# Performance work log

Hardware: AMD Instinct MI355X
Metric: run time of the kernel (lower is better)

Reference implementation:

```python
import jax, jax.numpy as jnp
import numpy as np

N, E = 20000, 320000
IN, OUT, H1, H2 = 256, 32, 8, 1
NEG_SLOPE = 0.2


def _gatv2(x, src, dst, Wsrc, bsrc, Wdst, bdst, attn, Wres, bres, heads, dout):
    n = x.shape[0]
    fs = (x @ Wsrc + bsrc).reshape(n, heads, dout)   # (N,H,D)
    fd = (x @ Wdst + bdst).reshape(n, heads, dout)   # (N,H,D)
    # GATv2: leaky_relu BEFORE the attention dot product
    e = jax.nn.leaky_relu(fs[src] + fd[dst], NEG_SLOPE)      # (E,H,D)
    logits = jnp.einsum('ehd,hd->eh', e, attn)               # (E,H)
    # edge softmax over destination-node segments
    m = jax.ops.segment_max(logits, dst, num_segments=n)     # (N,H)
    ex = jnp.exp(logits - m[dst])
    s = jax.ops.segment_sum(ex, dst, num_segments=n)         # (N,H)
    alpha = ex / s[dst]                                      # (E,H)
    msg = alpha[:, :, None] * fs[src]                        # (E,H,D)
    out = jax.ops.segment_sum(msg, dst, num_segments=n)      # (N,H,D)
    res = (x @ Wres + bres).reshape(n, heads, dout)          # residual (dims differ -> Linear)
    return out + res


def setup_inputs() -> dict:
    key = jax.random.key(0)
    ks = jax.random.split(key, 16)
    sc = lambda fin: 1.0 / np.sqrt(fin)
    d = {}
    d['x'] = jax.random.normal(ks[0], (N, IN), jnp.float32)
    d['src'] = jax.random.randint(ks[1], (E,), 0, N, jnp.int32)
    d['dst'] = jax.random.randint(ks[2], (E,), 0, N, jnp.int32)
    # layer 1: IN -> OUT*H1
    d['Wsrc1'] = jax.random.normal(ks[3], (IN, OUT * H1), jnp.float32) * sc(IN)
    d['bsrc1'] = jnp.zeros((OUT * H1,), jnp.float32)
    d['Wdst1'] = jax.random.normal(ks[4], (IN, OUT * H1), jnp.float32) * sc(IN)
    d['bdst1'] = jnp.zeros((OUT * H1,), jnp.float32)
    d['attn1'] = jax.random.normal(ks[5], (H1, OUT), jnp.float32) * sc(OUT)
    d['Wres1'] = jax.random.normal(ks[6], (IN, OUT * H1), jnp.float32) * sc(IN)
    d['bres1'] = jnp.zeros((OUT * H1,), jnp.float32)
    # layer 2: OUT*H1 -> OUT, 1 head
    D2 = OUT * H1
    d['Wsrc2'] = jax.random.normal(ks[7], (D2, OUT * H2), jnp.float32) * sc(D2)
    d['bsrc2'] = jnp.zeros((OUT * H2,), jnp.float32)
    d['Wdst2'] = jax.random.normal(ks[8], (D2, OUT * H2), jnp.float32) * sc(D2)
    d['bdst2'] = jnp.zeros((OUT * H2,), jnp.float32)
    d['attn2'] = jax.random.normal(ks[9], (H2, OUT), jnp.float32) * sc(OUT)
    d['Wres2'] = jax.random.normal(ks[10], (D2, OUT * H2), jnp.float32) * sc(D2)
    d['bres2'] = jnp.zeros((OUT * H2,), jnp.float32)
    return d


def reference(x, src, dst,
              Wsrc1, bsrc1, Wdst1, bdst1, attn1, Wres1, bres1,
              Wsrc2, bsrc2, Wdst2, bdst2, attn2, Wres2, bres2):
    y = _gatv2(x, src, dst, Wsrc1, bsrc1, Wdst1, bdst1, attn1, Wres1, bres1, H1, OUT)
    y = jax.nn.relu(y)                       # (N, 8, OUT)
    y = y.reshape(x.shape[0], -1)            # (N, 8*OUT)
    y = _gatv2(y, src, dst, Wsrc2, bsrc2, Wdst2, bdst2, attn2, Wres2, bres2, H2, OUT)
    return y                                  # (N, 1, OUT)
```

## Files before the change

### kernel.cpp

```cpp
#include <hip/hip_runtime.h>
#include <hip/hip_bf16.h>

#define N_NODES 20000
#define N_PAD   20096
#define N_EDGES 320000
#define D_IN    256
#define NEG     0.2f
#define MAXDEG  64
#define NSB     64
#define EPSB    5000
#define NBIN    313
#define LOG2E   1.4426950408889634f

typedef __attribute__((ext_vector_type(8))) short short8;
typedef __attribute__((ext_vector_type(4))) float f32x4;
typedef __attribute__((ext_vector_type(4))) unsigned short u16x4;

__device__ __forceinline__ unsigned short f2b(float f) {
    unsigned int u = __float_as_uint(f);
    unsigned int r = (u + 0x7FFFu + ((u >> 16) & 1u)) >> 16;
    return (unsigned short)r;
}
__device__ __forceinline__ float b2f(unsigned short u) {
    union { unsigned int i; float f; } v;
    v.i = ((unsigned int)u) << 16;
    return v.f;
}

__device__ __forceinline__ void gload16(const void* g, void* l) {
    __builtin_amdgcn_global_load_lds((const __attribute__((address_space(1))) void*)g,
                                     (__attribute__((address_space(3))) void*)l, 16, 0, 0);
}

#define PB1 2512
#define PB1B 2560
#define PB2 2656
#define PB3 2720
#define PREP_BLOCKS 2768
__global__ __launch_bounds__(256) void k_prep(
    const float* __restrict__ x, unsigned short* __restrict__ xb,
    const float* __restrict__ Ws1, const float* __restrict__ Wd1, const float* __restrict__ Wr1,
    unsigned short* __restrict__ wt,
    const float* __restrict__ Ws2, const float* __restrict__ Wd2, const float* __restrict__ Wr2,
    unsigned short* __restrict__ wt2,
    const int* __restrict__ dst, int* __restrict__ blockhist,
    unsigned short* __restrict__ yb)
{
    __shared__ float tl[64][65];
    __shared__ int hist[NBIN];
    int bid = blockIdx.x, tid = threadIdx.x;
    if (bid < PB1) {
        int i = bid * 256 + tid;
        int row = i >> 5, c8 = (i & 31) * 8;
        short8 v = {0, 0, 0, 0, 0, 0, 0, 0};
        if (row < N_NODES) {
            float4 a = *reinterpret_cast<const float4*>(x + (size_t)row * 256 + c8);
            float4 b = *reinterpret_cast<const float4*>(x + (size_t)row * 256 + c8 + 4);
            v[0] = (short)f2b(a.x); v[1] = (short)f2b(a.y); v[2] = (short)f2b(a.z); v[3] = (short)f2b(a.w);
            v[4] = (short)f2b(b.x); v[5] = (short)f2b(b.y); v[6] = (short)f2b(b.z); v[7] = (short)f2b(b.w);
        }
        *reinterpret_cast<short8*>(xb + (size_t)row * 256 + c8) = v;
    } else if (bid < PB1B) {
        int b = bid - PB1;
        int mat = b >> 4, tile = b & 15;
        int r0 = (tile >> 2) * 64;
        int c0 = (tile & 3) * 64;
        const float* W = (mat == 0) ? Ws1 : ((mat == 1) ? Wd1 : Wr1);
        int lane = tid & 63, grp = tid >> 6;
#pragma unroll
        for (int pass = 0; pass < 16; ++pass) {
            int kl = pass * 4 + grp;
            tl[kl][lane] = W[(size_t)(r0 + kl) * 256 + c0 + lane];
        }
        __syncthreads();
#pragma unroll
        for (int pass = 0; pass < 16; ++pass) {
            int nl = pass * 4 + grp;
            wt[(size_t)(mat * 256 + c0 + nl) * 256 + r0 + lane] = f2b(tl[lane][nl]);
        }
    } else if (bid < PB2) {
        int n = bid - PB1B, k = tid;
        const float* W = (n < 32) ? Ws2 : ((n < 64) ? Wd2 : Wr2);
        int c = n & 31;
        wt2[(size_t)n * 256 + (k ^ ((n & 7) << 3))] = f2b(W[(size_t)k * 32 + c]);
    } else if (bid < PB3) {
        int blk = bid - PB2;
        for (int b = tid; b < NBIN; b += 256) hist[b] = 0;
        __syncthreads();
        for (int it = 0; it < 20; ++it) {
            int li = it * 256 + tid;
            if (li < EPSB) atomicAdd(&hist[dst[blk * EPSB + li] >> 6], 1);
        }
        __syncthreads();
        for (int b = tid; b < NBIN; b += 256) blockhist[blk * NBIN + b] = hist[b];
    } else {
        int j = (bid - PB3) * 256 + tid;
        ((unsigned int*)(yb + (size_t)N_NODES * 256))[j] = 0u;
    }
}

__global__ __launch_bounds__(320) void k_pass3(
    const int* __restrict__ src, const int* __restrict__ dst,
    const int* __restrict__ blockhist,
    unsigned long long* __restrict__ sorted,
    int* __restrict__ binbase_g, int* __restrict__ bintotal_g)
{
    __shared__ int tmp[320];
    __shared__ int binbase[NBIN];
    __shared__ int rank[NBIN];
    int blk = blockIdx.x, tid = threadIdx.x;
    int mystart = 0, total = 0;
    if (tid < NBIN) {
        for (int b = 0; b < NSB; ++b) {
            int v = blockhist[b * NBIN + tid];
            total += v;
            if (b < blk) mystart += v;
        }
    }
    tmp[tid] = (tid < NBIN) ? total : 0;
    __syncthreads();
    for (int off = 1; off < 320; off <<= 1) {
        int v = (tid >= off) ? tmp[tid - off] : 0;
        __syncthreads();
        tmp[tid] += v;
        __syncthreads();
    }
    if (tid < NBIN) {
        int excl = tmp[tid] - total;
        binbase[tid] = excl;
        rank[tid] = mystart;
        if (blk == 0) { binbase_g[tid] = excl; bintotal_g[tid] = total; }
    }
    __syncthreads();
    for (int it = 0; it < 16; ++it) {
        int li = it * 320 + tid;
        if (li < EPSB) {
            int e = blk * EPSB + li;
            int d = dst[e];
            int b = d >> 6;
            int r = atomicAdd(&rank[b], 1);
            sorted[binbase[b] + r] = ((unsigned long long)(unsigned)d << 32) | (unsigned)src[e];
        }
    }
}

#define GEMM1_BLOCKS 1884
#define PASS4_BLOCKS 313
__global__ __launch_bounds__(256) void k_gemm_l1_mfma(
    const unsigned short* __restrict__ xb,
    const unsigned short* __restrict__ wt,
    const float* __restrict__ bs, const float* __restrict__ bd, const float* __restrict__ br,
    unsigned short* __restrict__ fs, unsigned short* __restrict__ fd, unsigned short* __restrict__ res,
    const unsigned long long* __restrict__ sorted,
    const int* __restrict__ binbase_g, const int* __restrict__ bintotal_g,
    int* __restrict__ colp, int* __restrict__ cnt)
{
    __shared__ __align__(16) unsigned short SH[12288];
    int t = threadIdx.x;
    int bid = blockIdx.x;

    if (bid >= GEMM1_BLOCKS) {
        int* ch = (int*)SH;
        int nb2 = bid - GEMM1_BLOCKS;
        if (t < 64) ch[t] = 0;
        __syncthreads();
        int base = binbase_g[nb2], tot = bintotal_g[nb2];
        for (int i = t; i < tot; i += 256) {
            unsigned long long p = sorted[base + i];
            int d = (int)(p >> 32);
            int s = (int)(p & 0xffffffffULL);
            int r = atomicAdd(&ch[d & 63], 1);
            if (r < MAXDEG) colp[(size_t)d * MAXDEG + r] = s;
        }
        __syncthreads();
        int node = nb2 * 64 + t;
        if (t < 64 && node < N_NODES) cnt[node] = ch[t];
        return;
    }

    int lane = t & 63, w = t >> 6;
    const int q = 235, r = 4;
    int xcd = bid & 7, slot = bid >> 3;
    int wg = (xcd < r ? xcd * (q + 1) : r * (q + 1) + (xcd - r) * q) + slot;
    int mb = wg / 6, nb = wg % 6;
    int row0 = mb * 64;
    int which = nb >> 1;
    int col0 = (nb & 1) * 128;
    int ncol0 = nb * 128;
    unsigned short* out = (which == 0) ? fs : ((which == 1) ? fd : res);
    const float* bias   = (which == 0) ? bs : ((which == 1) ? bd : br);

    auto stage = [&](int buf, int k0) {
        char* base = (char*)SH + buf * 12288;
        {
            int c = t, row = c >> 2, kc = (c & 3) * 8;
            gload16(xb + (size_t)(row0 + row) * 256 + k0 + kc, base + c * 16);
        }
#pragma unroll
        for (int r2 = 0; r2 < 2; r2++) {
            int c = r2 * 256 + t, row = c >> 2, kc = (c & 3) * 8;
            gload16(wt + (size_t)(ncol0 + row) * 256 + k0 + kc, base + 4096 + c * 16);
        }
    };

    f32x4 acc[4][2] = {};

    stage(0, 0);
    __syncthreads();
    int cur = 0;
#pragma unroll
    for (int it = 0; it < 8; ++it) {
        if (it < 7) stage(cur ^ 1, (it + 1) * 32);
        const char* Ab = (const char*)SH + cur * 12288;
        const char* Bb = Ab + 4096;
        short8 a[4], b[2];
#pragma unroll
        for (int m = 0; m < 4; m++)
            a[m] = *reinterpret_cast<const short8*>(Ab + ((m * 16 + (lane & 15)) * 64 + (lane >> 4) * 16));
#pragma unroll
        for (int n = 0; n < 2; n++)
            b[n] = *reinterpret_cast<const short8*>(Bb + ((w * 32 + n * 16 + (lane & 15)) * 64 + (lane >> 4) * 16));
#pragma unroll
        for (int m = 0; m < 4; m++)
#pragma unroll
            for (int n = 0; n < 2; n++)
                acc[m][n] = __builtin_amdgcn_mfma_f32_16x16x32_bf16(a[m], b[n], acc[m][n], 0, 0, 0);
        __syncthreads();
        cur ^= 1;
    }

    int cgrp = lane >> 4, ccol = lane & 15;
    float bvals[2];
#pragma unroll
    for (int n = 0; n < 2; n++) bvals[n] = bias[col0 + w * 32 + n * 16 + ccol];

#pragma unroll
    for (int m = 0; m < 4; m++)
#pragma unroll
        for (int n = 0; n < 2; n++)
#pragma unroll
            for (int q2 = 0; q2 < 4; q2++) {
                int lr = m * 16 + cgrp * 4 + q2;
                int cb = (w * 32 + n * 16 + ccol) * 2;
                int addr = lr * 256 + (cb ^ (cgrp << 5));
                *(unsigned short*)((char*)SH + addr) = f2b(acc[m][n][q2] + bvals[n]);
            }
    __syncthreads();
#pragma unroll
    for (int it = 0; it < 4; it++) {
        int lr = it * 16 + (t >> 4);
        int cb = (t & 15) * 16;
        short8 v = *(const short8*)((const char*)SH + (lr * 256 + (cb ^ (((lr >> 2) & 3) << 5))));
        int gr = row0 + lr;
        if (gr < N_NODES)
            *reinterpret_cast<short8*>(out + (size_t)gr * 256 + col0 + (t & 15) * 8) = v;
    }
}

__global__ __launch_bounds__(64) void k_gather_l1(
    const int* __restrict__ cnt, const int* __restrict__ colp,
    const unsigned short* __restrict__ fs1, const unsigned short* __restrict__ fd1,
    const unsigned short* __restrict__ res1, const float* __restrict__ attn1,
    unsigned short* __restrict__ y)
{
    __shared__ int slds[MAXDEG + 8];
    int n = blockIdx.x;
    int l = threadIdx.x;
    int deg = cnt[n];
    if (deg > MAXDEG) deg = MAXDEG;
    slds[l] = (l < deg) ? colp[(size_t)n * MAXDEG + l] : 0;
    if (l < 8) slds[MAXDEG + l] = 0;
    __syncthreads();

    u16x4 fdv4 = *reinterpret_cast<const u16x4*>(fd1 + (size_t)n * 256 + l * 4);
    float fdv[4] = {b2f(fdv4[0]), b2f(fdv4[1]), b2f(fdv4[2]), b2f(fdv4[3])};
    float4 attv = *reinterpret_cast<const float4*>(attn1 + l * 4);
    float att[4] = {attv.x * LOG2E, attv.y * LOG2E, attv.z * LOG2E, attv.w * LOG2E};

    float mA = -1e30f, sA = 0.f, aA0 = 0.f, aA1 = 0.f, aA2 = 0.f, aA3 = 0.f;
    float mB = -1e30f, sB = 0.f, aB0 = 0.f, aB1 = 0.f, aB2 = 0.f, aB3 = 0.f;

    u16x4 fA  = *reinterpret_cast<const u16x4*>(fs1 + (size_t)slds[0] * 256 + l * 4);
    u16x4 fB  = *reinterpret_cast<const u16x4*>(fs1 + (size_t)slds[1] * 256 + l * 4);
    u16x4 fA2 = *reinterpret_cast<const u16x4*>(fs1 + (size_t)slds[2] * 256 + l * 4);
    u16x4 fB2 = *reinterpret_cast<const u16x4*>(fs1 + (size_t)slds[3] * 256 + l * 4);

    int idx = 0;
    for (; idx + 1 < deg; idx += 2) {
        u16x4 vA = fA, vB = fB;
        fA = fA2; fB = fB2;
        fA2 = *reinterpret_cast<const u16x4*>(fs1 + (size_t)slds[idx + 4] * 256 + l * 4);
        fB2 = *reinterpret_cast<const u16x4*>(fs1 + (size_t)slds[idx + 5] * 256 + l * 4);

        float xa0 = b2f(vA[0]), xa1 = b2f(vA[1]), xa2 = b2f(vA[2]), xa3 = b2f(vA[3]);
        float ta0 = xa0 + fdv[0]; ta0 = fmaxf(ta0, NEG * ta0);
        float ta1 = xa1 + fdv[1]; ta1 = fmaxf(ta1, NEG * ta1);
        float ta2 = xa2 + fdv[2]; ta2 = fmaxf(ta2, NEG * ta2);
        float ta3 = xa3 + fdv[3]; ta3 = fmaxf(ta3, NEG * ta3);
        float pA = ta0 * att[0] + ta1 * att[1] + ta2 * att[2] + ta3 * att[3];

        float xb0 = b2f(vB[0]), xb1 = b2f(vB[1]), xb2 = b2f(vB[2]), xb3 = b2f(vB[3]);
        float tb0 = xb0 + fdv[0]; tb0 = fmaxf(tb0, NEG * tb0);
        float tb1 = xb1 + fdv[1]; tb1 = fmaxf(tb1, NEG * tb1);
        float tb2 = xb2 + fdv[2]; tb2 = fmaxf(tb2, NEG * tb2);
        float tb3 = xb3 + fdv[3]; tb3 = fmaxf(tb3, NEG * tb3);
        float pB = tb0 * att[0] + tb1 * att[1] + tb2 * att[2] + tb3 * att[3];

        pA += __shfl_xor(pA, 1); pB += __shfl_xor(pB, 1);
        pA += __shfl_xor(pA, 2); pB += __shfl_xor(pB, 2);
        pA += __shfl_xor(pA, 4); pB += __shfl_xor(pB, 4);

        float mnA = fmaxf(mA, pA);
        float eA  = exp2f(pA - mnA);
        float scA = exp2f(mA - mnA);
        sA = sA * scA + eA;
        aA0 = aA0 * scA + eA * xa0;
        aA1 = aA1 * scA + eA * xa1;
        aA2 = aA2 * scA + eA * xa2;
        aA3 = aA3 * scA + eA * xa3;
        mA = mnA;

        float mnB = fmaxf(mB, pB);
        float eB  = exp2f(pB - mnB);
        float scB = exp2f(mB - mnB);
        sB = sB * scB + eB;
        aB0 = aB0 * scB + eB * xb0;
        aB1 = aB1 * scB + eB * xb1;
        aB2 = aB2 * scB + eB * xb2;
        aB3 = aB3 * scB + eB * xb3;
        mB = mnB;
    }
    if (idx < deg) {
        float xa0 = b2f(fA[0]), xa1 = b2f(fA[1]), xa2 = b2f(fA[2]), xa3 = b2f(fA[3]);
        float ta0 = xa0 + fdv[0]; ta0 = fmaxf(ta0, NEG * ta0);
        float ta1 = xa1 + fdv[1]; ta1 = fmaxf(ta1, NEG * ta1);
        float ta2 = xa2 + fdv[2]; ta2 = fmaxf(ta2, NEG * ta2);
        float ta3 = xa3 + fdv[3]; ta3 = fmaxf(ta3, NEG * ta3);
        float pA = ta0 * att[0] + ta1 * att[1] + ta2 * att[2] + ta3 * att[3];
        pA += __shfl_xor(pA, 1);
        pA += __shfl_xor(pA, 2);
        pA += __shfl_xor(pA, 4);
        float mnA = fmaxf(mA, pA);
        float eA  = exp2f(pA - mnA);
        float scA = exp2f(mA - mnA);
        sA = sA * scA + eA;
        aA0 = aA0 * scA + eA * xa0;
        aA1 = aA1 * scA + eA * xa1;
        aA2 = aA2 * scA + eA * xa2;
        aA3 = aA3 * scA + eA * xa3;
        mA = mnA;
    }
    float mn = fmaxf(mA, mB);
    float scA = exp2f(mA - mn), scB = exp2f(mB - mn);
    float s  = sA * scA + sB * scB;
    float a0 = aA0 * scA + aB0 * scB;
    float a1 = aA1 * scA + aB1 * scB;
    float a2 = aA2 * scA + aB2 * scB;
    float a3 = aA3 * scA + aB3 * scB;

    u16x4 rv4 = *reinterpret_cast<const u16x4*>(res1 + (size_t)n * 256 + l * 4);
    float inv = (s > 0.f) ? 1.f / s : 0.f;
    u16x4 o;
    o[0] = f2b(fmaxf(a0 * inv + b2f(rv4[0]), 0.f));
    o[1] = f2b(fmaxf(a1 * inv + b2f(rv4[1]), 0.f));
    o[2] = f2b(fmaxf(a2 * inv + b2f(rv4[2]), 0.f));
    o[3] = f2b(fmaxf(a3 * inv + b2f(rv4[3]), 0.f));
    *reinterpret_cast<u16x4*>(y + (size_t)n * 256 + l * 4) = o;
}

__global__ __launch_bounds__(256) void k_gemm_l2_mfma(
    const unsigned short* __restrict__ yb,
    const unsigned short* __restrict__ wt2,
    const float* __restrict__ bs, const float* __restrict__ bd, const float* __restrict__ br,
    unsigned short* __restrict__ fs2, unsigned short* __restrict__ fd2, unsigned short* __restrict__ res2)
{
    __shared__ __align__(16) unsigned short Bs[96 * 256];
    __shared__ __align__(16) unsigned short As[2][64 * 32];
    int t = threadIdx.x;
    int lane = t & 63, w = t >> 6;
    int row0 = blockIdx.x * 64;

    auto stage_a = [&](int buf, int k0) {
        int c = t;
        int row = c >> 2, kc = (c & 3) * 8;
        gload16(yb + (size_t)(row0 + row) * 256 + k0 + kc, (char*)As[buf] + c * 16);
    };

#pragma unroll
    for (int i = 0; i < 12; i++) {
        int c = i * 256 + t;
        gload16(wt2 + (size_t)c * 8, (char*)Bs + (size_t)c * 16);
    }
    stage_a(0, 0);
    __syncthreads();

    f32x4 acc[6] = {};
    int arow0 = w * 16;
    int cur = 0;

#pragma unroll
    for (int it = 0; it < 8; ++it) {
        if (it < 7) stage_a(cur ^ 1, (it + 1) * 32);
        short8 a = *reinterpret_cast<const short8*>((const char*)As[cur] + ((arow0 + (lane & 15)) * 64 + (lane >> 4) * 16));
        short8 b[6];
#pragma unroll
        for (int n = 0; n < 6; n++) {
            int brow = n * 16 + (lane & 15);
            int kbyte = (it * 32 + (lane >> 4) * 8) * 2;
            b[n] = *reinterpret_cast<const short8*>((const char*)Bs + (brow * 512 + (kbyte ^ ((brow & 7) << 4))));
        }
#pragma unroll
        for (int n = 0; n < 6; n++)
            acc[n] = __builtin_amdgcn_mfma_f32_16x16x32_bf16(a, b[n], acc[n], 0, 0, 0);
        __syncthreads();
        cur ^= 1;
    }

    int cgrp = lane >> 4, ccol = lane & 15;
#pragma unroll
    for (int n = 0; n < 6; n++) {
        int which = n >> 1;
        int cc = (n & 1) * 16 + ccol;
        unsigned short* out = (which == 0) ? fs2 : ((which == 1) ? fd2 : res2);
        const float* bias   = (which == 0) ? bs  : ((which == 1) ? bd  : br);
        float bv = bias[cc];
        int rbase = row0 + arow0 + cgrp * 4;
#pragma unroll
        for (int q2 = 0; q2 < 4; q2++) {
            int rr = rbase + q2;
            if (rr < N_NODES) out[(size_t)rr * 32 + cc] = f2b(acc[n][q2] + bv);
        }
    }
}

__global__ __launch_bounds__(64) void k_gather_l2(
    const int* __restrict__ cnt, const int* __restrict__ colp,
    const unsigned short* __restrict__ fs2, const unsigned short* __restrict__ fd2,
    const unsigned short* __restrict__ res2, const float* __restrict__ attn2,
    float* __restrict__ out)
{
    __shared__ int slds[MAXDEG + 8];
    int n = blockIdx.x;
    int l = threadIdx.x;
    int d = l & 31, h = l >> 5;
    int deg = cnt[n];
    if (deg > MAXDEG) deg = MAXDEG;
    slds[l] = (l < deg) ? colp[(size_t)n * MAXDEG + l] : 0;
    if (l < 8) slds[MAXDEG + l] = 0;
    __syncthreads();

    float fdv = b2f(fd2[(size_t)n * 32 + d]);
    float att = attn2[d] * LOG2E;
    float m = -1e30f, s = 0.f, acc = 0.f;
    float fv_next = b2f(fs2[(size_t)slds[h] * 32 + d]);
    for (int i = h; i < deg; i += 2) {
        float fv = fv_next;
        fv_next = b2f(fs2[(size_t)slds[i + 2] * 32 + d]);
        float t0 = fv + fdv; t0 = fmaxf(t0, NEG * t0);
        float p = t0 * att;
        p += __shfl_xor(p, 1);
        p += __shfl_xor(p, 2);
        p += __shfl_xor(p, 4);
        p += __shfl_xor(p, 8);
        p += __shfl_xor(p, 16);
        float mn = fmaxf(m, p);
        float e  = exp2f(p - mn);
        float sc = exp2f(m - mn);
        s = s * sc + e;
        acc = acc * sc + e * fv;
        m = mn;
    }
    float mo = __shfl_xor(m, 32);
    float mstar = fmaxf(m, mo);
    float myc = exp2f(m - mstar);
    float sp = s * myc, ap = acc * myc;
    float st = sp + __shfl_xor(sp, 32);
    float at = ap + __shfl_xor(ap, 32);
    if (l < 32) {
        float rv = b2f(res2[(size_t)n * 32 + d]);
        float inv = (st > 0.f) ? 1.f / st : 0.f;
        out[(size_t)n * 32 + d] = at * inv + rv;
    }
}

extern "C" void kernel_launch(void* const* d_in, const int* in_sizes, int n_in,
                              void* d_out, int out_size, void* d_ws, size_t ws_size,
                              hipStream_t stream)
{
    const float* x   = (const float*)d_in[0];
    const int*   src = (const int*)d_in[1];
    const int*   dst = (const int*)d_in[2];
    const float* Ws1 = (const float*)d_in[3];
    const float* bs1 = (const float*)d_in[4];
    const float* Wd1 = (const float*)d_in[5];
    const float* bd1 = (const float*)d_in[6];
    const float* at1 = (const float*)d_in[7];
    const float* Wr1 = (const float*)d_in[8];
    const float* br1 = (const float*)d_in[9];
    const float* Ws2 = (const float*)d_in[10];
    const float* bs2 = (const float*)d_in[11];
    const float* Wd2 = (const float*)d_in[12];
    const float* bd2 = (const float*)d_in[13];
    const float* at2 = (const float*)d_in[14];
    const float* Wr2 = (const float*)d_in[15];
    const float* br2 = (const float*)d_in[16];
    float* out = (float*)d_out;

    char* w = (char*)d_ws;
    size_t off = 0;
    auto alloc = [&](size_t bytes) { void* p = w + off; off += (bytes + 255) & ~(size_t)255; return p; };
    int*   cnt       = (int*)  alloc((size_t)N_NODES * 4);
    int*   colp      = (int*)  alloc((size_t)N_NODES * MAXDEG * 4);
    int*   blockhist = (int*)  alloc((size_t)NSB * NBIN * 4);
    int*   bintotal  = (int*)  alloc((size_t)NBIN * 4);
    int*   binbase   = (int*)  alloc((size_t)NBIN * 4);
    unsigned long long* sorted = (unsigned long long*)alloc((size_t)N_EDGES * 8);
    unsigned short* fs1 = (unsigned short*)alloc((size_t)N_NODES * 256 * 2);
    unsigned short* fd1 = (unsigned short*)alloc((size_t)N_NODES * 256 * 2);
    unsigned short* res1= (unsigned short*)alloc((size_t)N_NODES * 256 * 2);
    unsigned short* fs2 = (unsigned short*)alloc((size_t)N_NODES * 32 * 2);
    unsigned short* fd2 = (unsigned short*)alloc((size_t)N_NODES * 32 * 2);
    unsigned short* res2= (unsigned short*)alloc((size_t)N_NODES * 32 * 2);
    unsigned short* xb  = (unsigned short*)alloc((size_t)N_PAD * 256 * 2);
    unsigned short* yb  = (unsigned short*)alloc((size_t)N_PAD * 256 * 2);
    unsigned short* wt  = (unsigned short*)alloc((size_t)768 * 256 * 2);
    unsigned short* wt2 = (unsigned short*)alloc((size_t)96 * 256 * 2);
    (void)ws_size; (void)in_sizes; (void)n_in; (void)out_size;

    k_prep<<<PREP_BLOCKS, 256, 0, stream>>>(x, xb, Ws1, Wd1, Wr1, wt, Ws2, Wd2, Wr2, wt2,
                                            dst, blockhist, yb);
    k_pass3<<<NSB, 320, 0, stream>>>(src, dst, blockhist, sorted, binbase, bintotal);
    k_gemm_l1_mfma<<<GEMM1_BLOCKS + PASS4_BLOCKS, 256, 0, stream>>>(
        xb, wt, bs1, bd1, br1, fs1, fd1, res1, sorted, binbase, bintotal, colp, cnt);
    k_gather_l1<<<N_NODES, 64, 0, stream>>>(cnt, colp, fs1, fd1, res1, at1, yb);
    k_gemm_l2_mfma<<<N_PAD / 64, 256, 0, stream>>>(yb, wt2, bs2, bd2, br2, fs2, fd2, res2);
    k_gather_l2<<<N_NODES, 64, 0, stream>>>(cnt, colp, fs2, fd2, res2, at2, out);
}
```

Baseline: 108.6 us.

## Split layer-1 gather into head-pair groups with grouped fs1 layout

The layer-1 GEMM now writes fs1 in a group-major layout (4 groups of 64 columns, each a contiguous N×64 slab). The gather kernel launches a 2D grid with one block per node and column group, and processes four edges at once per wave (16 lanes per edge). Partial online-softmax states are merged across lanes with shuffles. The aim is more parallelism and better cache locality for the random source-row gathers, at the cost of four times as many blocks, redundant index loads per block, and dropping the explicit software prefetch.

```diff
diff --git a/kernel.cpp b/kernel.cpp
--- a/kernel.cpp
+++ b/kernel.cpp
@@ -252,8 +252,13 @@
         int cb = (t & 15) * 16;
         short8 v = *(const short8*)((const char*)SH + (lr * 256 + (cb ^ (((lr >> 2) & 3) << 5))));
         int gr = row0 + lr;
-        if (gr < N_NODES)
-            *reinterpret_cast<short8*>(out + (size_t)gr * 256 + col0 + (t & 15) * 8) = v;
+        if (gr < N_NODES) {
+            int gc = col0 + (t & 15) * 8;
+            if (which == 0)
+                *reinterpret_cast<short8*>(fs + ((size_t)(gc >> 6) * N_NODES + gr) * 64 + (gc & 63)) = v;
+            else
+                *reinterpret_cast<short8*>(out + (size_t)gr * 256 + gc) = v;
+        }
     }
 }
 
@@ -263,109 +268,76 @@
     const unsigned short* __restrict__ res1, const float* __restrict__ attn1,
     unsigned short* __restrict__ y)
 {
-    __shared__ int slds[MAXDEG + 8];
-    int n = blockIdx.x;
+    __shared__ int slds[MAXDEG + 4];
+    int n = blockIdx.x, g = blockIdx.y;
     int l = threadIdx.x;
+    int esub = l >> 4, li = l & 15;
     int deg = cnt[n];
     if (deg > MAXDEG) deg = MAXDEG;
     slds[l] = (l < deg) ? colp[(size_t)n * MAXDEG + l] : 0;
-    if (l < 8) slds[MAXDEG + l] = 0;
-    __syncthreads();
-
-    u16x4 fdv4 = *reinterpret_cast<const u16x4*>(fd1 + (size_t)n * 256 + l * 4);
-    float fdv[4] = {b2f(fdv4[0]), b2f(fdv4[1]), b2f(fdv4[2]), b2f(fdv4[3])};
-    float4 attv = *reinterpret_cast<const float4*>(attn1 + l * 4);
-    float att[4] = {attv.x * LOG2E, attv.y * LOG2E, attv.z * LOG2E, attv.w * LOG2E};
-
-    float mA = -1e30f, sA = 0.f, aA0 = 0.f, aA1 = 0.f, aA2 = 0.f, aA3 = 0.f;
-    float mB = -1e30f, sB = 0.f, aB0 = 0.f, aB1 = 0.f, aB2 = 0.f, aB3 = 0.f;
-
-    u16x4 fA  = *reinterpret_cast<const u16x4*>(fs1 + (size_t)slds[0] * 256 + l * 4);
-    u16x4 fB  = *reinterpret_cast<const u16x4*>(fs1 + (size_t)slds[1] * 256 + l * 4);
-    u16x4 fA2 = *reinterpret_cast<const u16x4*>(fs1 + (size_t)slds[2] * 256 + l * 4);
-    u16x4 fB2 = *reinterpret_cast<const u16x4*>(fs1 + (size_t)slds[3] * 256 + l * 4);
-
-    int idx = 0;
-    for (; idx + 1 < deg; idx += 2) {
-        u16x4 vA = fA, vB = fB;
-        fA = fA2; fB = fB2;
-        fA2 = *reinterpret_cast<const u16x4*>(fs1 + (size_t)slds[idx + 4] * 256 + l * 4);
-        fB2 = *reinterpret_cast<const u16x4*>(fs1 + (size_t)slds[idx + 5] * 256 + l * 4);
-
-        float xa0 = b2f(vA[0]), xa1 = b2f(vA[1]), xa2 = b2f(vA[2]), xa3 = b2f(vA[3]);
-        float ta0 = xa0 + fdv[0]; ta0 = fmaxf(ta0, NEG * ta0);
-        float ta1 = xa1 + fdv[1]; ta1 = fmaxf(ta1, NEG * ta1);
-        float ta2 = xa2 + fdv[2]; ta2 = fmaxf(ta2, NEG * ta2);
-        float ta3 = xa3 + fdv[3]; ta3 = fmaxf(ta3, NEG * ta3);
-        float pA = ta0 * att[0] + ta1 * att[1] + ta2 * att[2] + ta3 * att[3];
-
-        float xb0 = b2f(vB[0]), xb1 = b2f(vB[1]), xb2 = b2f(vB[2]), xb3 = b2f(vB[3]);
-        float tb0 = xb0 + fdv[0]; tb0 = fmaxf(tb0, NEG * tb0);
-        float tb1 = xb1 + fdv[1]; tb1 = fmaxf(tb1, NEG * tb1);
-        float tb2 = xb2 + fdv[2]; tb2 = fmaxf(tb2, NEG * tb2);
-        float tb3 = xb3 + fdv[3]; tb3 = fmaxf(tb3, NEG * tb3);
-        float pB = tb0 * att[0] + tb1 * att[1] + tb2 * att[2] + tb3 * att[3];
-
-        pA += __shfl_xor(pA, 1); pB += __shfl_xor(pB, 1);
-        pA += __shfl_xor(pA, 2); pB += __shfl_xor(pB, 2);
-        pA += __shfl_xor(pA, 4); pB += __shfl_xor(pB, 4);
-
-        float mnA = fmaxf(mA, pA);
-        float eA  = exp2f(pA - mnA);
-        float scA = exp2f(mA - mnA);
-        sA = sA * scA + eA;
-        aA0 = aA0 * scA + eA * xa0;
-        aA1 = aA1 * scA + eA * xa1;
-        aA2 = aA2 * scA + eA * xa2;
-        aA3 = aA3 * scA + eA * xa3;
-        mA = mnA;
-
-        float mnB = fmaxf(mB, pB);
-        float eB  = exp2f(pB - mnB);
-        float scB = exp2f(mB - mnB);
-        sB = sB * scB + eB;
-        aB0 = aB0 * scB + eB * xb0;
-        aB1 = aB1 * scB + eB * xb1;
-        aB2 = aB2 * scB + eB * xb2;
-        aB3 = aB3 * scB + eB * xb3;
-        mB = mnB;
-    }
-    if (idx < deg) {
-        float xa0 = b2f(fA[0]), xa1 = b2f(fA[1]), xa2 = b2f(fA[2]), xa3 = b2f(fA[3]);
-        float ta0 = xa0 + fdv[0]; ta0 = fmaxf(ta0, NEG * ta0);
-        float ta1 = xa1 + fdv[1]; ta1 = fmaxf(ta1, NEG * ta1);
-        float ta2 = xa2 + fdv[2]; ta2 = fmaxf(ta2, NEG * ta2);
-        float ta3 = xa3 + fdv[3]; ta3 = fmaxf(ta3, NEG * ta3);
-        float pA = ta0 * att[0] + ta1 * att[1] + ta2 * att[2] + ta3 * att[3];
-        pA += __shfl_xor(pA, 1);
-        pA += __shfl_xor(pA, 2);
-        pA += __shfl_xor(pA, 4);
-        float mnA = fmaxf(mA, pA);
-        float eA  = exp2f(pA - mnA);
-        float scA = exp2f(mA - mnA);
-        sA = sA * scA + eA;
-        aA0 = aA0 * scA + eA * xa0;
-        aA1 = aA1 * scA + eA * xa1;
-        aA2 = aA2 * scA + eA * xa2;
-        aA3 = aA3 * scA + eA * xa3;
-        mA = mnA;
-    }
-    float mn = fmaxf(mA, mB);
-    float scA = exp2f(mA - mn), scB = exp2f(mB - mn);
-    float s  = sA * scA + sB * scB;
-    float a0 = aA0 * scA + aB0 * scB;
-    float a1 = aA1 * scA + aB1 * scB;
-    float a2 = aA2 * scA + aB2 * scB;
-    float a3 = aA3 * scA + aB3 * scB;
-
-    u16x4 rv4 = *reinterpret_cast<const u16x4*>(res1 + (size_t)n * 256 + l * 4);
-    float inv = (s > 0.f) ? 1.f / s : 0.f;
-    u16x4 o;
-    o[0] = f2b(fmaxf(a0 * inv + b2f(rv4[0]), 0.f));
-    o[1] = f2b(fmaxf(a1 * inv + b2f(rv4[1]), 0.f));
-    o[2] = f2b(fmaxf(a2 * inv + b2f(rv4[2]), 0.f));
-    o[3] = f2b(fmaxf(a3 * inv + b2f(rv4[3]), 0.f));
-    *reinterpret_cast<u16x4*>(y + (size_t)n * 256 + l * 4) = o;
+    if (l < 4) slds[MAXDEG + l] = 0;
+    __syncthreads();
+
+    const unsigned short* fsg = fs1 + (size_t)g * N_NODES * 64;
+    u16x4 fdv4 = *reinterpret_cast<const u16x4*>(fd1 + (size_t)n * 256 + g * 64 + li * 4);
+    float fdv0 = b2f(fdv4[0]), fdv1 = b2f(fdv4[1]), fdv2 = b2f(fdv4[2]), fdv3 = b2f(fdv4[3]);
+    float4 attv = *reinterpret_cast<const float4*>(attn1 + g * 64 + li * 4);
+    float at0 = attv.x * LOG2E, at1 = attv.y * LOG2E, at2 = attv.z * LOG2E, at3 = attv.w * LOG2E;
+
+    float m = -1e30f, s = 0.f, a0 = 0.f, a1 = 0.f, a2 = 0.f, a3 = 0.f;
+    int iters = (deg + 3) >> 2;
+    for (int it = 0; it < iters; ++it) {
+        int i = it * 4 + esub;
+        int srcn = slds[i];
+        u16x4 fv4 = *reinterpret_cast<const u16x4*>(fsg + (size_t)srcn * 64 + li * 4);
+        float x0 = b2f(fv4[0]), x1 = b2f(fv4[1]), x2 = b2f(fv4[2]), x3 = b2f(fv4[3]);
+        float t0 = x0 + fdv0; t0 = fmaxf(t0, NEG * t0);
+        float t1 = x1 + fdv1; t1 = fmaxf(t1, NEG * t1);
+        float t2 = x2 + fdv2; t2 = fmaxf(t2, NEG * t2);
+        float t3 = x3 + fdv3; t3 = fmaxf(t3, NEG * t3);
+        float p = t0 * at0 + t1 * at1 + t2 * at2 + t3 * at3;
+        p += __shfl_xor(p, 1);
+        p += __shfl_xor(p, 2);
+        p += __shfl_xor(p, 4);
+        bool valid = (i < deg);
+        p = valid ? p : -1e30f;
+        float mn = fmaxf(m, p);
+        float e  = valid ? exp2f(p - mn) : 0.f;
+        float sc = exp2f(m - mn);
+        s = s * sc + e;
+        a0 = a0 * sc + e * x0;
+        a1 = a1 * sc + e * x1;
+        a2 = a2 * sc + e * x2;
+        a3 = a3 * sc + e * x3;
+        m = mn;
+    }
+#pragma unroll
+    for (int mask = 16; mask <= 32; mask <<= 1) {
+        float mo = __shfl_xor(m, mask);
+        float so = __shfl_xor(s, mask);
+        float b0 = __shfl_xor(a0, mask);
+        float b1 = __shfl_xor(a1, mask);
+        float b2 = __shfl_xor(a2, mask);
+        float b3 = __shfl_xor(a3, mask);
+        float mn = fmaxf(m, mo);
+        float c1 = exp2f(m - mn), c2 = exp2f(mo - mn);
+        s  = s * c1 + so * c2;
+        a0 = a0 * c1 + b0 * c2;
+        a1 = a1 * c1 + b1 * c2;
+        a2 = a2 * c1 + b2 * c2;
+        a3 = a3 * c1 + b3 * c2;
+        m = mn;
+    }
+    if (l < 16) {
+        u16x4 rv4 = *reinterpret_cast<const u16x4*>(res1 + (size_t)n * 256 + g * 64 + li * 4);
+        float inv = (s > 0.f) ? 1.f / s : 0.f;
+        u16x4 o;
+        o[0] = f2b(fmaxf(a0 * inv + b2f(rv4[0]), 0.f));
+        o[1] = f2b(fmaxf(a1 * inv + b2f(rv4[1]), 0.f));
+        o[2] = f2b(fmaxf(a2 * inv + b2f(rv4[2]), 0.f));
+        o[3] = f2b(fmaxf(a3 * inv + b2f(rv4[3]), 0.f));
+        *reinterpret_cast<u16x4*>(y + (size_t)n * 256 + g * 64 + li * 4) = o;
+    }
 }
 
 __global__ __launch_bounds__(256) void k_gemm_l2_mfma(
@@ -515,7 +487,7 @@
     int*   bintotal  = (int*)  alloc((size_t)NBIN * 4);
     int*   binbase   = (int*)  alloc((size_t)NBIN * 4);
     unsigned long long* sorted = (unsigned long long*)alloc((size_t)N_EDGES * 8);
-    unsigned short* fs1 = (unsigned short*)alloc((size_t)N_NODES * 256 * 2);
+    unsigned short* fs1 = (unsigned short*)alloc((size_t)4 * N_NODES * 64 * 2);
     unsigned short* fd1 = (unsigned short*)alloc((size_t)N_NODES * 256 * 2);
     unsigned short* res1= (unsigned short*)alloc((size_t)N_NODES * 256 * 2);
     unsigned short* fs2 = (unsigned short*)alloc((size_t)N_NODES * 32 * 2);
@@ -532,7 +504,7 @@
     k_pass3<<<NSB, 320, 0, stream>>>(src, dst, blockhist, sorted, binbase, bintotal);
     k_gemm_l1_mfma<<<GEMM1_BLOCKS + PASS4_BLOCKS, 256, 0, stream>>>(
         xb, wt, bs1, bd1, br1, fs1, fd1, res1, sorted, binbase, bintotal, colp, cnt);
-    k_gather_l1<<<N_NODES, 64, 0, stream>>>(cnt, colp, fs1, fd1, res1, at1, yb);
+    k_gather_l1<<<dim3(N_NODES, 4), 64, 0, stream>>>(cnt, colp, fs1, fd1, res1, at1, yb);
     k_gemm_l2_mfma<<<N_PAD / 64, 256, 0, stream>>>(yb, wt2, bs2, bd2, br2, fs2, fd2, res2);
     k_gather_l2<<<N_NODES, 64, 0, stream>>>(cnt, colp, fs2, fd2, res2, at2, out);
 }
```

Result: slower. 123.0 us (+13.2%).
